# Performance work log

Measured on AMD Instinct MI355X. Metric: run time of the kernel, lower is better.

## Reference

```python
import jax, jax.numpy as jnp
import numpy as np

HEAD_DIM = 64
KERNEL_SIZE = 3
DILATION = 1
SCALE = HEAD_DIM ** (-0.5)

B, C, H, W = 8, 384, 64, 64


def _unfold(x, ks, dilation):
    """Mimic nn.Unfold(ks, dilation, padding=dilation*(ks-1)//2, stride=1).
    x: [B, C, H, W] -> [B, C, ks*ks, H, W] (zero-padded, kernel positions row-major)."""
    b, c, h, w = x.shape
    pad = dilation * (ks - 1) // 2
    xp = jnp.pad(x, ((0, 0), (0, 0), (pad, pad), (pad, pad)))
    patches = [xp[:, :, i * dilation:i * dilation + h, j * dilation:j * dilation + w]
               for i in range(ks) for j in range(ks)]
    return jnp.stack(patches, axis=2)  # [B, C, kk, H, W]


def setup_inputs() -> dict:
    key = jax.random.key(0)
    kq, kk, kv = jax.random.split(key, 3)
    q = jax.random.normal(kq, (B, C, H, W), dtype=jnp.float32)
    k = jax.random.normal(kk, (B, C, H, W), dtype=jnp.float32)
    v = jax.random.normal(kv, (B, C, H, W), dtype=jnp.float32)
    return {"q": q, "k": k, "v": v}


def reference(q, k, v):
    b, c, h, w = q.shape
    nh = c // HEAD_DIM
    kk = KERNEL_SIZE * KERNEL_SIZE
    n = h * w
    # q: [B, nh, hd, N]
    qh = q.reshape(b, nh, HEAD_DIM, n)
    # unfolded k, v: [B, nh, hd, kk, N]
    ku = _unfold(k, KERNEL_SIZE, DILATION).reshape(b, nh, HEAD_DIM, kk, n)
    vu = _unfold(v, KERNEL_SIZE, DILATION).reshape(b, nh, HEAD_DIM, kk, n)
    # scores per pixel: [B, nh, N, kk]
    attn = jnp.einsum('bhdn,bhdkn->bhnk', qh, ku) * SCALE
    attn = jax.nn.softmax(attn, axis=-1)
    # out: [B, nh, N, hd]
    out = jnp.einsum('bhnk,bhdkn->bhnd', attn, vu)
    # [B, N, nh, hd] -> [B, H, W, C]
    x = out.transpose(0, 2, 1, 3).reshape(b, h, w, c)
    return x
```

## Files before the change

### kernel.cpp

```cpp
#include <hip/hip_runtime.h>

#define BB 8
#define CC 384
#define HH 64
#define WW 64
#define NH 6
#define HD 64
#define PLANE (HH*WW)
#define QKSCALE 0.125f
#define CH_B  (PLANE*4)
#define CHUNK_B (8*CH_B)

typedef float f32x4 __attribute__((ext_vector_type(4)));
typedef int   i32x4 __attribute__((ext_vector_type(4)));

__device__ __forceinline__ i32x4 make_srsrc(const void* p) {
  union { unsigned long long a; int w[2]; } u; u.a = (unsigned long long)p;
  i32x4 r; r.x = u.w[0]; r.y = u.w[1]; r.z = -1 ; r.w = 0x00020000;
  return r;
}

__device__ __forceinline__ void bl(float& dst, i32x4 rsrc, int voff, int soff) {
  asm volatile("buffer_load_dword %0, %1, %2, %3 offen"
               : "=v"(dst) : "v"(voff), "s"(rsrc), "s"(soff));
}

__device__ __forceinline__ void issue_q8(float (&qb)[8], i32x4 rq, int voq) {
#pragma unroll
  for (int dd = 0; dd < 8; ++dd) bl(qb[dd], rq, voq, dd * CH_B);
}
__device__ __forceinline__ void issue_r24(float (&kb)[24], i32x4 rk, int vo0, int vo1, int vo2) {
#pragma unroll
  for (int dd = 0; dd < 8; ++dd) bl(kb[0 * 8 + dd], rk, vo0, dd * CH_B);
#pragma unroll
  for (int dd = 0; dd < 8; ++dd) bl(kb[1 * 8 + dd], rk, vo1, dd * CH_B);
#pragma unroll
  for (int dd = 0; dd < 8; ++dd) bl(kb[2 * 8 + dd], rk, vo2, dd * CH_B);
}

__global__ __launch_bounds__(256, 2) void dilate_attn_kernel(
    const float* __restrict__ qg, const float* __restrict__ kg,
    const float* __restrict__ vg, float* __restrict__ outg) {
  const int blk  = (blockIdx.x % 8) * 96 + (blockIdx.x / 8);
  const int nyb  = HH / 4;
  const int y0   = (blk % nyb) * 4;
  const int bh   = blk / nyb;
  const int head = bh % NH;
  const int b    = bh / NH;
  const int lane = threadIdx.x & 63;
  const int warp = threadIdx.x >> 6;
  const int y = y0 + warp;
  const int x = lane;

  const int laneL = (lane - 1) & 63;
  const int laneR = (lane + 1) & 63;

  const i32x4 rq = make_srsrc(qg);
  const i32x4 rk = make_srsrc(kg);
  const i32x4 rv = make_srsrc(vg);

  const int slab4 = (b * CC + head * HD) * (PLANE * 4);
  const int voq = slab4 + (y * WW + x) * 4;

  int vor[3];
  float m[9];
#pragma unroll
  for (int r = 0; r < 3; ++r) {
    const int yy = y + r - 1;
    const int yc = min(max(yy, 0), HH - 1);
    vor[r] = slab4 + (yc * WW + x) * 4;
    const bool rowok = (yy >= 0) && (yy < HH);
#pragma unroll
    for (int dx = 0; dx < 3; ++dx) {
      const int xx = x + dx - 1;
      m[r * 3 + dx] = (rowok && xx >= 0 && xx < WW) ? 1.0f : 0.0f;
    }
  }

  float t[9];
#pragma unroll
  for (int i = 0; i < 9; ++i) t[i] = 0.0f;

  float qb[2][8], kb[2][24];
  issue_q8(qb[0], rq, voq);
  issue_r24(kb[0], rk, vor[0], vor[1], vor[2]);

#pragma unroll
  for (int c = 0; c < 8; ++c) {
    const int cur = c & 1, nxt = cur ^ 1;
    if (c < 7) {
      issue_q8(qb[nxt], rq, voq + (c + 1) * CHUNK_B);
      issue_r24(kb[nxt], rk, vor[0] + (c + 1) * CHUNK_B,
                             vor[1] + (c + 1) * CHUNK_B,
                             vor[2] + (c + 1) * CHUNK_B);
    }
    if (c < 7) { asm volatile("s_waitcnt vmcnt(56)" ::: "memory"); }
    else       { asm volatile("s_waitcnt vmcnt(24)" ::: "memory"); }
    __builtin_amdgcn_sched_barrier(0);
    float qm[8], qp[8];
#pragma unroll
    for (int dd = 0; dd < 8; ++dd) {
      qm[dd] = __shfl(qb[cur][dd], laneL);
      qp[dd] = __shfl(qb[cur][dd], laneR);
    }
    if (c < 7) { asm volatile("s_waitcnt vmcnt(32)" ::: "memory"); }
    else       { asm volatile("s_waitcnt vmcnt(0)"  ::: "memory"); }
    __builtin_amdgcn_sched_barrier(0);
#pragma unroll
    for (int dd = 0; dd < 8; ++dd) {
#pragma unroll
      for (int r = 0; r < 3; ++r) {
        const float kc = kb[cur][r * 8 + dd];
        t[r * 3 + 0] = fmaf(kc, qp[dd], t[r * 3 + 0]);
        t[r * 3 + 1] = fmaf(kc, qb[cur][dd], t[r * 3 + 1]);
        t[r * 3 + 2] = fmaf(kc, qm[dd], t[r * 3 + 2]);
      }
    }
  }

  float vb[2][24];
  issue_r24(vb[0], rv, vor[0], vor[1], vor[2]);

  float s[9];
#pragma unroll
  for (int i = 0; i < 9; ++i) {
    const int dx = (i % 3) - 1;
    s[i] = __shfl(t[i], (lane + dx) & 63) * m[i] * QKSCALE;
  }
  float mx = s[0];
#pragma unroll
  for (int i = 1; i < 9; ++i) mx = fmaxf(mx, s[i]);
  float sum = 0.0f;
#pragma unroll
  for (int i = 0; i < 9; ++i) { s[i] = __expf(s[i] - mx); sum += s[i]; }
  const float inv = 1.0f / sum;
#pragma unroll
  for (int i = 0; i < 9; ++i) s[i] = s[i] * inv * m[i];

  float P[9];
#pragma unroll
  for (int i = 0; i < 9; ++i) {
    const int dx = (i % 3) - 1;
    P[i] = __shfl(s[i], (lane - dx) & 63);
  }

  float* outp = outg + ((long)((b * HH + y) * WW + x)) * CC + head * HD;

#pragma unroll
  for (int c = 0; c < 8; ++c) {
    const int cur = c & 1, nxt = cur ^ 1;
    if (c < 7) issue_r24(vb[nxt], rv, vor[0] + (c + 1) * CHUNK_B,
                                      vor[1] + (c + 1) * CHUNK_B,
                                      vor[2] + (c + 1) * CHUNK_B);
    if (c < 7) { asm volatile("s_waitcnt vmcnt(24)" ::: "memory"); }
    else       { asm volatile("s_waitcnt vmcnt(0)"  ::: "memory"); }
    __builtin_amdgcn_sched_barrier(0);

#pragma unroll
    for (int g = 0; g < 2; ++g) {
      f32x4 ov;
#pragma unroll
      for (int j = 0; j < 4; ++j) {
        const int dd = g * 4 + j;
        float cm = 0.f, cz = 0.f, cp = 0.f;
#pragma unroll
        for (int r = 0; r < 3; ++r) {
          const float vc = vb[cur][r * 8 + dd];
          cm = fmaf(P[r * 3 + 0], vc, cm);
          cz = fmaf(P[r * 3 + 1], vc, cz);
          cp = fmaf(P[r * 3 + 2], vc, cp);
        }
        ov[j] = cz + __shfl(cm, laneL) + __shfl(cp, laneR);
      }
      *reinterpret_cast<f32x4*>(outp + c * 8 + g * 4) = ov;
    }
  }
}

extern "C" void kernel_launch(void* const* d_in, const int* in_sizes, int n_in,
                              void* d_out, int out_size, void* d_ws, size_t ws_size,
                              hipStream_t stream) {
  const float* q = (const float*)d_in[0];
  const float* k = (const float*)d_in[1];
  const float* v = (const float*)d_in[2];
  float* out = (float*)d_out;
  const int blocks = BB * NH * (HH / 4);
  dilate_attn_kernel<<<blocks, 256, 0, stream>>>(q, k, v, out);
}
```

Measured before the change: 41.47 us.

## Split PV channel loop across two waves per row, doubling block count

Each block now covers 2 rows instead of 4. Two waves share each row: both redundantly compute the full QK scores and softmax, then each handles half of the 64 value channels in the PV stage. Grid size doubles and launch bounds request 4 blocks per CU, aiming for more parallelism and latency hiding in the PV phase. The cost is duplicated Q/K loads and score arithmetic, plus tighter register limits that may cause spills.

```diff
diff --git a/kernel.cpp b/kernel.cpp
--- a/kernel.cpp
+++ b/kernel.cpp
@@ -10,6 +10,8 @@
 #define QKSCALE 0.125f
 #define CH_B  (PLANE*4)
 #define CHUNK_B (8*CH_B)
+#define NCHUNK_QK 8
+#define NCHUNK_PV 4
 
 typedef float f32x4 __attribute__((ext_vector_type(4)));
 typedef int   i32x4 __attribute__((ext_vector_type(4)));
@@ -38,18 +40,19 @@
   for (int dd = 0; dd < 8; ++dd) bl(kb[2 * 8 + dd], rk, vo2, dd * CH_B);
 }
 
-__global__ __launch_bounds__(256, 2) void dilate_attn_kernel(
+__global__ __launch_bounds__(256, 4) void dilate_attn_kernel(
     const float* __restrict__ qg, const float* __restrict__ kg,
     const float* __restrict__ vg, float* __restrict__ outg) {
-  const int blk  = (blockIdx.x % 8) * 96 + (blockIdx.x / 8);
-  const int nyb  = HH / 4;
-  const int y0   = (blk % nyb) * 4;
-  const int bh   = blk / nyb;
+  const int blk  = (blockIdx.x % 8) * 192 + (blockIdx.x / 8);
+  const int y0   = (blk % 32) * 2;
+  const int bh   = blk / 32;
   const int head = bh % NH;
   const int b    = bh / NH;
   const int lane = threadIdx.x & 63;
-  const int warp = threadIdx.x >> 6;
-  const int y = y0 + warp;
+  const int w    = threadIdx.x >> 6;
+  const int yloc = w >> 1;
+  const int h    = w & 1;
+  const int y = y0 + yloc;
   const int x = lane;
 
   const int laneL = (lane - 1) & 63;
@@ -86,16 +89,16 @@
   issue_r24(kb[0], rk, vor[0], vor[1], vor[2]);
 
 #pragma unroll
-  for (int c = 0; c < 8; ++c) {
+  for (int c = 0; c < NCHUNK_QK; ++c) {
     const int cur = c & 1, nxt = cur ^ 1;
-    if (c < 7) {
+    if (c < NCHUNK_QK - 1) {
       issue_q8(qb[nxt], rq, voq + (c + 1) * CHUNK_B);
       issue_r24(kb[nxt], rk, vor[0] + (c + 1) * CHUNK_B,
                              vor[1] + (c + 1) * CHUNK_B,
                              vor[2] + (c + 1) * CHUNK_B);
     }
-    if (c < 7) { asm volatile("s_waitcnt vmcnt(56)" ::: "memory"); }
-    else       { asm volatile("s_waitcnt vmcnt(24)" ::: "memory"); }
+    if (c < NCHUNK_QK - 1) { asm volatile("s_waitcnt vmcnt(56)" ::: "memory"); }
+    else                   { asm volatile("s_waitcnt vmcnt(24)" ::: "memory"); }
     __builtin_amdgcn_sched_barrier(0);
     float qm[8], qp[8];
 #pragma unroll
@@ -103,8 +106,8 @@
       qm[dd] = __shfl(qb[cur][dd], laneL);
       qp[dd] = __shfl(qb[cur][dd], laneR);
     }
-    if (c < 7) { asm volatile("s_waitcnt vmcnt(32)" ::: "memory"); }
-    else       { asm volatile("s_waitcnt vmcnt(0)"  ::: "memory"); }
+    if (c < NCHUNK_QK - 1) { asm volatile("s_waitcnt vmcnt(32)" ::: "memory"); }
+    else                   { asm volatile("s_waitcnt vmcnt(0)"  ::: "memory"); }
     __builtin_amdgcn_sched_barrier(0);
 #pragma unroll
     for (int dd = 0; dd < 8; ++dd) {
@@ -118,8 +121,11 @@
     }
   }
 
+  const int vv0 = vor[0] + h * 32 * CH_B;
+  const int vv1 = vor[1] + h * 32 * CH_B;
+  const int vv2 = vor[2] + h * 32 * CH_B;
   float vb[2][24];
-  issue_r24(vb[0], rv, vor[0], vor[1], vor[2]);
+  issue_r24(vb[0], rv, vv0, vv1, vv2);
 
   float s[9];
 #pragma unroll
@@ -144,16 +150,17 @@
     P[i] = __shfl(s[i], (lane - dx) & 63);
   }
 
-  float* outp = outg + ((long)((b * HH + y) * WW + x)) * CC + head * HD;
+  float* outp = outg + ((long)((b * HH + y) * WW + x)) * CC + head * HD + h * 32;
 
 #pragma unroll
-  for (int c = 0; c < 8; ++c) {
+  for (int c = 0; c < NCHUNK_PV; ++c) {
     const int cur = c & 1, nxt = cur ^ 1;
-    if (c < 7) issue_r24(vb[nxt], rv, vor[0] + (c + 1) * CHUNK_B,
-                                      vor[1] + (c + 1) * CHUNK_B,
-                                      vor[2] + (c + 1) * CHUNK_B);
-    if (c < 7) { asm volatile("s_waitcnt vmcnt(24)" ::: "memory"); }
-    else       { asm volatile("s_waitcnt vmcnt(0)"  ::: "memory"); }
+    if (c < NCHUNK_PV - 1)
+      issue_r24(vb[nxt], rv, vv0 + (c + 1) * CHUNK_B,
+                             vv1 + (c + 1) * CHUNK_B,
+                             vv2 + (c + 1) * CHUNK_B);
+    if (c < NCHUNK_PV - 1) { asm volatile("s_waitcnt vmcnt(24)" ::: "memory"); }
+    else                   { asm volatile("s_waitcnt vmcnt(0)"  ::: "memory"); }
     __builtin_amdgcn_sched_barrier(0);
 
 #pragma unroll
@@ -184,6 +191,6 @@
   const float* k = (const float*)d_in[1];
   const float* v = (const float*)d_in[2];
   float* out = (float*)d_out;
-  const int blocks = BB * NH * (HH / 4);
+  const int blocks = BB * NH * (HH / 2);
   dilate_attn_kernel<<<blocks, 256, 0, stream>>>(q, k, v, out);
 }
```

Result: slower. 48.11 us (+16.0%).

## Vectorize loads to dwordx4 with lane-group channel split and LDS transpose

Applied to the files above, without the earlier changes.

Reassigns work so each lane owns 4 consecutive x pixels and one channel group of a 16-lane quarter-wave, which allows 128-bit buffer loads instead of scalar dword loads. QK partial sums are reduced across the four channel groups with xor shuffles, and softmax runs per pixel in registers. Output is transposed through LDS so each lane writes contiguous channels. The change cuts the number of memory instructions and raises the occupancy target, at the cost of extra shuffles, redundant softmax work across lane groups, LDS traffic, and register pressure from the 9x4 accumulators.

```diff
diff --git a/kernel.cpp b/kernel.cpp
--- a/kernel.cpp
+++ b/kernel.cpp
@@ -9,7 +9,6 @@
 #define PLANE (HH*WW)
 #define QKSCALE 0.125f
 #define CH_B  (PLANE*4)
-#define CHUNK_B (8*CH_B)
 
 typedef float f32x4 __attribute__((ext_vector_type(4)));
 typedef int   i32x4 __attribute__((ext_vector_type(4)));
@@ -20,160 +19,196 @@
   return r;
 }
 
-__device__ __forceinline__ void bl(float& dst, i32x4 rsrc, int voff, int soff) {
-  asm volatile("buffer_load_dword %0, %1, %2, %3 offen"
+__device__ __forceinline__ void blx4(f32x4& dst, i32x4 rsrc, int voff, int soff) {
+  asm volatile("buffer_load_dwordx4 %0, %1, %2, %3 offen"
                : "=v"(dst) : "v"(voff), "s"(rsrc), "s"(soff));
 }
 
-__device__ __forceinline__ void issue_q8(float (&qb)[8], i32x4 rq, int voq) {
-#pragma unroll
-  for (int dd = 0; dd < 8; ++dd) bl(qb[dd], rq, voq, dd * CH_B);
-}
-__device__ __forceinline__ void issue_r24(float (&kb)[24], i32x4 rk, int vo0, int vo1, int vo2) {
-#pragma unroll
-  for (int dd = 0; dd < 8; ++dd) bl(kb[0 * 8 + dd], rk, vo0, dd * CH_B);
-#pragma unroll
-  for (int dd = 0; dd < 8; ++dd) bl(kb[1 * 8 + dd], rk, vo1, dd * CH_B);
-#pragma unroll
-  for (int dd = 0; dd < 8; ++dd) bl(kb[2 * 8 + dd], rk, vo2, dd * CH_B);
-}
-
-__global__ __launch_bounds__(256, 2) void dilate_attn_kernel(
+__global__ __launch_bounds__(256, 3) void dilate_attn_kernel(
     const float* __restrict__ qg, const float* __restrict__ kg,
     const float* __restrict__ vg, float* __restrict__ outg) {
   const int blk  = (blockIdx.x % 8) * 96 + (blockIdx.x / 8);
-  const int nyb  = HH / 4;
-  const int y0   = (blk % nyb) * 4;
-  const int bh   = blk / nyb;
+  const int y0   = (blk % 16) * 4;
+  const int bh   = blk / 16;
   const int head = bh % NH;
   const int b    = bh / NH;
   const int lane = threadIdx.x & 63;
   const int warp = threadIdx.x >> 6;
   const int y = y0 + warp;
-  const int x = lane;
-
-  const int laneL = (lane - 1) & 63;
-  const int laneR = (lane + 1) & 63;
+  const int g = lane >> 4;
+  const int u = lane & 15;
+
+  const int laneM = (lane & 48) | ((u + 15) & 15);
+  const int laneP = (lane & 48) | ((u + 1) & 15);
 
   const i32x4 rq = make_srsrc(qg);
   const i32x4 rk = make_srsrc(kg);
   const i32x4 rv = make_srsrc(vg);
 
-  const int slab4 = (b * CC + head * HD) * (PLANE * 4);
-  const int voq = slab4 + (y * WW + x) * 4;
-
-  int vor[3];
-  float m[9];
+  const int slab4 = (b * CC + head * HD) * (PLANE * 4) + g * CH_B;
+  const int voq = slab4 + (y * WW + 4 * u) * 4;
+
+  int vok[3]; float rowm[3];
 #pragma unroll
   for (int r = 0; r < 3; ++r) {
     const int yy = y + r - 1;
     const int yc = min(max(yy, 0), HH - 1);
-    vor[r] = slab4 + (yc * WW + x) * 4;
-    const bool rowok = (yy >= 0) && (yy < HH);
-#pragma unroll
-    for (int dx = 0; dx < 3; ++dx) {
-      const int xx = x + dx - 1;
-      m[r * 3 + dx] = (rowok && xx >= 0 && xx < WW) ? 1.0f : 0.0f;
-    }
-  }
-
-  float t[9];
-#pragma unroll
-  for (int i = 0; i < 9; ++i) t[i] = 0.0f;
-
-  float qb[2][8], kb[2][24];
-  issue_q8(qb[0], rq, voq);
-  issue_r24(kb[0], rk, vor[0], vor[1], vor[2]);
+    vok[r] = slab4 + (yc * WW + 4 * u) * 4;
+    rowm[r] = (yy >= 0 && yy < HH) ? 1.0f : 0.0f;
+  }
+  const float eL = (u == 0)  ? 0.0f : 1.0f;
+  const float eR = (u == 15) ? 0.0f : 1.0f;
+
+  float t[9][4];
+#pragma unroll
+  for (int i = 0; i < 9; ++i)
+#pragma unroll
+    for (int j = 0; j < 4; ++j) t[i][j] = 0.0f;
+
+  f32x4 qb[2][2], kb[2][6];
+  blx4(qb[0][0], rq, voq, 0 * CH_B);
+  blx4(qb[0][1], rq, voq, 4 * CH_B);
+#pragma unroll
+  for (int r = 0; r < 3; ++r)
+#pragma unroll
+    for (int ci = 0; ci < 2; ++ci)
+      blx4(kb[0][r * 2 + ci], rk, vok[r], (4 * ci) * CH_B);
 
 #pragma unroll
   for (int c = 0; c < 8; ++c) {
     const int cur = c & 1, nxt = cur ^ 1;
     if (c < 7) {
-      issue_q8(qb[nxt], rq, voq + (c + 1) * CHUNK_B);
-      issue_r24(kb[nxt], rk, vor[0] + (c + 1) * CHUNK_B,
-                             vor[1] + (c + 1) * CHUNK_B,
-                             vor[2] + (c + 1) * CHUNK_B);
-    }
-    if (c < 7) { asm volatile("s_waitcnt vmcnt(56)" ::: "memory"); }
-    else       { asm volatile("s_waitcnt vmcnt(24)" ::: "memory"); }
+      const int cb = (c + 1) * 8;
+      blx4(qb[nxt][0], rq, voq, (cb + 0) * CH_B);
+      blx4(qb[nxt][1], rq, voq, (cb + 4) * CH_B);
+#pragma unroll
+      for (int r = 0; r < 3; ++r)
+#pragma unroll
+        for (int ci = 0; ci < 2; ++ci)
+          blx4(kb[nxt][r * 2 + ci], rk, vok[r], (cb + 4 * ci) * CH_B);
+    }
+    if (c < 7) { asm volatile("s_waitcnt vmcnt(8)" ::: "memory"); }
+    else       { asm volatile("s_waitcnt vmcnt(0)" ::: "memory"); }
     __builtin_amdgcn_sched_barrier(0);
-    float qm[8], qp[8];
-#pragma unroll
-    for (int dd = 0; dd < 8; ++dd) {
-      qm[dd] = __shfl(qb[cur][dd], laneL);
-      qp[dd] = __shfl(qb[cur][dd], laneR);
-    }
-    if (c < 7) { asm volatile("s_waitcnt vmcnt(32)" ::: "memory"); }
-    else       { asm volatile("s_waitcnt vmcnt(0)"  ::: "memory"); }
-    __builtin_amdgcn_sched_barrier(0);
-#pragma unroll
-    for (int dd = 0; dd < 8; ++dd) {
+
+#pragma unroll
+    for (int ci = 0; ci < 2; ++ci) {
+      const f32x4 qv = qb[cur][ci];
 #pragma unroll
       for (int r = 0; r < 3; ++r) {
-        const float kc = kb[cur][r * 8 + dd];
-        t[r * 3 + 0] = fmaf(kc, qp[dd], t[r * 3 + 0]);
-        t[r * 3 + 1] = fmaf(kc, qb[cur][dd], t[r * 3 + 1]);
-        t[r * 3 + 2] = fmaf(kc, qm[dd], t[r * 3 + 2]);
+        const f32x4 kv = kb[cur][r * 2 + ci];
+        const float km1 = __shfl(kv[3], laneM);
+        const float kp4 = __shfl(kv[0], laneP);
+        t[r*3+0][0] = fmaf(qv[0], km1,  t[r*3+0][0]);
+        t[r*3+0][1] = fmaf(qv[1], kv[0], t[r*3+0][1]);
+        t[r*3+0][2] = fmaf(qv[2], kv[1], t[r*3+0][2]);
+        t[r*3+0][3] = fmaf(qv[3], kv[2], t[r*3+0][3]);
+        t[r*3+1][0] = fmaf(qv[0], kv[0], t[r*3+1][0]);
+        t[r*3+1][1] = fmaf(qv[1], kv[1], t[r*3+1][1]);
+        t[r*3+1][2] = fmaf(qv[2], kv[2], t[r*3+1][2]);
+        t[r*3+1][3] = fmaf(qv[3], kv[3], t[r*3+1][3]);
+        t[r*3+2][0] = fmaf(qv[0], kv[1], t[r*3+2][0]);
+        t[r*3+2][1] = fmaf(qv[1], kv[2], t[r*3+2][1]);
+        t[r*3+2][2] = fmaf(qv[2], kv[3], t[r*3+2][2]);
+        t[r*3+2][3] = fmaf(qv[3], kp4,  t[r*3+2][3]);
       }
     }
   }
 
-  float vb[2][24];
-  issue_r24(vb[0], rv, vor[0], vor[1], vor[2]);
-
-  float s[9];
-#pragma unroll
-  for (int i = 0; i < 9; ++i) {
-    const int dx = (i % 3) - 1;
-    s[i] = __shfl(t[i], (lane + dx) & 63) * m[i] * QKSCALE;
-  }
-  float mx = s[0];
-#pragma unroll
-  for (int i = 1; i < 9; ++i) mx = fmaxf(mx, s[i]);
-  float sum = 0.0f;
-#pragma unroll
-  for (int i = 0; i < 9; ++i) { s[i] = __expf(s[i] - mx); sum += s[i]; }
-  const float inv = 1.0f / sum;
-#pragma unroll
-  for (int i = 0; i < 9; ++i) s[i] = s[i] * inv * m[i];
-
-  float P[9];
-#pragma unroll
-  for (int i = 0; i < 9; ++i) {
-    const int dx = (i % 3) - 1;
-    P[i] = __shfl(s[i], (lane - dx) & 63);
-  }
-
-  float* outp = outg + ((long)((b * HH + y) * WW + x)) * CC + head * HD;
+  f32x4 vb[2][6];
+#pragma unroll
+  for (int r = 0; r < 3; ++r)
+#pragma unroll
+    for (int ci = 0; ci < 2; ++ci)
+      blx4(vb[0][r * 2 + ci], rv, vok[r], (4 * ci) * CH_B);
+
+#pragma unroll
+  for (int i = 0; i < 9; ++i)
+#pragma unroll
+    for (int j = 0; j < 4; ++j) {
+      t[i][j] += __shfl_xor(t[i][j], 16);
+      t[i][j] += __shfl_xor(t[i][j], 32);
+    }
+
+  float p[9][4];
+#pragma unroll
+  for (int j = 0; j < 4; ++j) {
+    float sj[9];
+#pragma unroll
+    for (int r = 0; r < 3; ++r)
+#pragma unroll
+      for (int d = 0; d < 3; ++d)
+        sj[r * 3 + d] = t[r * 3 + d][j] * rowm[r] * QKSCALE;
+    if (j == 0) { sj[0] *= eL; sj[3] *= eL; sj[6] *= eL; }
+    if (j == 3) { sj[2] *= eR; sj[5] *= eR; sj[8] *= eR; }
+    float mx = sj[0];
+#pragma unroll
+    for (int i = 1; i < 9; ++i) mx = fmaxf(mx, sj[i]);
+    float sum = 0.0f;
+#pragma unroll
+    for (int i = 0; i < 9; ++i) { sj[i] = __expf(sj[i] - mx); sum += sj[i]; }
+    const float inv = 1.0f / sum;
+#pragma unroll
+    for (int r = 0; r < 3; ++r)
+#pragma unroll
+      for (int d = 0; d < 3; ++d)
+        p[r * 3 + d][j] = sj[r * 3 + d] * inv * rowm[r];
+    if (j == 0) { p[0][0] *= eL; p[3][0] *= eL; p[6][0] *= eL; }
+    if (j == 3) { p[2][3] *= eR; p[5][3] *= eR; p[8][3] *= eR; }
+  }
+
+  __shared__ float ldsT[4][576];
+  float* ldsw = ldsT[warp];
+  float* outp = outg + ((long)((b * HH + y) * WW + lane)) * CC + head * HD;
 
 #pragma unroll
   for (int c = 0; c < 8; ++c) {
     const int cur = c & 1, nxt = cur ^ 1;
-    if (c < 7) issue_r24(vb[nxt], rv, vor[0] + (c + 1) * CHUNK_B,
-                                      vor[1] + (c + 1) * CHUNK_B,
-                                      vor[2] + (c + 1) * CHUNK_B);
-    if (c < 7) { asm volatile("s_waitcnt vmcnt(24)" ::: "memory"); }
-    else       { asm volatile("s_waitcnt vmcnt(0)"  ::: "memory"); }
+    if (c < 7) {
+      const int cb = (c + 1) * 8;
+#pragma unroll
+      for (int r = 0; r < 3; ++r)
+#pragma unroll
+        for (int ci = 0; ci < 2; ++ci)
+          blx4(vb[nxt][r * 2 + ci], rv, vok[r], (cb + 4 * ci) * CH_B);
+    }
+    if (c < 7) { asm volatile("s_waitcnt vmcnt(6)" ::: "memory"); }
+    else       { asm volatile("s_waitcnt vmcnt(0)" ::: "memory"); }
     __builtin_amdgcn_sched_barrier(0);
 
-#pragma unroll
-    for (int g = 0; g < 2; ++g) {
-      f32x4 ov;
-#pragma unroll
-      for (int j = 0; j < 4; ++j) {
-        const int dd = g * 4 + j;
-        float cm = 0.f, cz = 0.f, cp = 0.f;
-#pragma unroll
-        for (int r = 0; r < 3; ++r) {
-          const float vc = vb[cur][r * 8 + dd];
-          cm = fmaf(P[r * 3 + 0], vc, cm);
-          cz = fmaf(P[r * 3 + 1], vc, cz);
-          cp = fmaf(P[r * 3 + 2], vc, cp);
-        }
-        ov[j] = cz + __shfl(cm, laneL) + __shfl(cp, laneR);
+    float o[2][4];
+#pragma unroll
+    for (int ci = 0; ci < 2; ++ci)
+#pragma unroll
+      for (int j = 0; j < 4; ++j) o[ci][j] = 0.0f;
+
+#pragma unroll
+    for (int ci = 0; ci < 2; ++ci)
+#pragma unroll
+      for (int r = 0; r < 3; ++r) {
+        const f32x4 vv = vb[cur][r * 2 + ci];
+        const float vm1 = __shfl(vv[3], laneM);
+        const float vp4 = __shfl(vv[0], laneP);
+        o[ci][0] += p[r*3+0][0]*vm1  + p[r*3+1][0]*vv[0] + p[r*3+2][0]*vv[1];
+        o[ci][1] += p[r*3+0][1]*vv[0] + p[r*3+1][1]*vv[1] + p[r*3+2][1]*vv[2];
+        o[ci][2] += p[r*3+0][2]*vv[1] + p[r*3+1][2]*vv[2] + p[r*3+2][2]*vv[3];
+        o[ci][3] += p[r*3+0][3]*vv[2] + p[r*3+1][3]*vv[3] + p[r*3+2][3]*vp4;
       }
-      *reinterpret_cast<f32x4*>(outp + c * 8 + g * 4) = ov;
-    }
+
+#pragma unroll
+    for (int ci = 0; ci < 2; ++ci)
+#pragma unroll
+      for (int j = 0; j < 4; ++j)
+        ldsw[(4 * u + j) * 9 + 4 * ci + g] = o[ci][j];
+
+    f32x4 o0, o1;
+#pragma unroll
+    for (int c2 = 0; c2 < 4; ++c2) {
+      o0[c2] = ldsw[lane * 9 + c2];
+      o1[c2] = ldsw[lane * 9 + 4 + c2];
+    }
+    *reinterpret_cast<f32x4*>(outp + c * 8)     = o0;
+    *reinterpret_cast<f32x4*>(outp + c * 8 + 4) = o1;
   }
 }
 
```

Measured after the change: 43.30 us. +4.4%, slower.
